# Kernel optimization log

Hardware: AMD Instinct MI355X
Metric: run time of the kernel (lower is better)

Reference implementation:

```python
import jax, jax.numpy as jnp
import numpy as np

B, IN, H, M = 16384, 512, 512, 4096


def setup_inputs() -> dict:
    key = jax.random.key(0)
    ks = jax.random.split(key, 8)
    s_in = 1.0 / np.sqrt(IN + H)
    return {
        "input_tensor": jax.random.normal(ks[0], (B, IN), jnp.float32),
        "hidden": jax.random.normal(ks[1], (B, H), jnp.float32),
        "cell": jax.random.normal(ks[2], (B, H), jnp.float32),
        # fused gate weights: columns = [input, forget, cell, output] gates
        "W_gates": jax.random.normal(ks[3], (IN + H, 4 * H), jnp.float32) * s_in,
        "b_gates": jnp.zeros((4 * H,), jnp.float32),
        "W_attn": jax.random.normal(ks[4], (H, M), jnp.float32) / np.sqrt(H),
        "b_attn": jnp.zeros((M,), jnp.float32),
        "memory_matrix": jax.random.normal(ks[5], (M, H), jnp.float32) * np.sqrt(2.0 / (M + H)),
    }


def reference(input_tensor, hidden, cell, W_gates, b_gates, W_attn, b_attn, memory_matrix):
    combined = jnp.concatenate([input_tensor, hidden], axis=1)        # (B, IN+H)
    gates = combined @ W_gates + b_gates                              # (B, 4H)
    i_g, f_g, c_g, o_g = jnp.split(gates, 4, axis=1)
    i_g = jax.nn.sigmoid(i_g)
    f_g = jax.nn.sigmoid(f_g)
    c_g = jnp.tanh(c_g)
    o_g = jax.nn.sigmoid(o_g)
    attn = jax.nn.softmax(hidden @ W_attn + b_attn, axis=1)           # (B, M)
    memory_read = attn @ memory_matrix                                # (B, H)
    new_cell = f_g * cell + i_g * c_g + 0.1 * memory_read
    new_hidden = o_g * jnp.tanh(new_cell)
    return (new_hidden, new_cell, attn)
```

## Files before the change

### kernel.cpp

```cpp
#include <hip/hip_runtime.h>
#include <hip/hip_bf16.h>
#include <math.h>

typedef __bf16 bf16_t;
typedef bf16_t bf16x8 __attribute__((ext_vector_type(8)));
typedef float  f32x4  __attribute__((ext_vector_type(4)));

static constexpr int Bn = 16384;
static constexpr int Hn = 512;

__device__ __forceinline__ float sigm(float x) { return 1.0f / (1.0f + __expf(-x)); }

typedef __attribute__((address_space(3))) void lds_void;
typedef const __attribute__((address_space(1))) void gl_void;

__device__ __forceinline__ void glds16(const void* g, void* l) {
    __builtin_amdgcn_global_load_lds((gl_void*)g, (lds_void*)l, 16, 0, 0);
}

__global__ void prologue(const float* __restrict__ inp, const float* __restrict__ hid,
                         bf16_t* __restrict__ comb,
                         const float* __restrict__ Wg, bf16_t* __restrict__ WgT,
                         const float* __restrict__ Wa, bf16_t* __restrict__ WaT,
                         const float* __restrict__ Mem, bf16_t* __restrict__ MemT)
{
    int b = blockIdx.x;
    if (b < 8192) {
        size_t t = (size_t)b * blockDim.x + threadIdx.x;
        size_t r = t >> 7;
        int c8 = (int)(t & 127);
        const float* src = (c8 < 64) ? (inp + r * 512 + c8 * 8) : (hid + r * 512 + (c8 - 64) * 8);
        float4 a = ((const float4*)src)[0];
        float4 bb = ((const float4*)src)[1];
        bf16x8 o;
        o[0] = (bf16_t)a.x; o[1] = (bf16_t)a.y; o[2] = (bf16_t)a.z; o[3] = (bf16_t)a.w;
        o[4] = (bf16_t)bb.x; o[5] = (bf16_t)bb.y; o[6] = (bf16_t)bb.z; o[7] = (bf16_t)bb.w;
        *(bf16x8*)(comb + t * 8) = o;
        return;
    }
    b -= 8192;
    __shared__ float tile[32][33];
    const float* src; bf16_t* dst; int R, C, gx;
    if (b < 2048)      { src = Wg;  dst = WgT;  R = 1024; C = 2048; gx = 64; }
    else if (b < 4096) { b -= 2048; src = Wa;  dst = WaT;  R = 512;  C = 4096; gx = 128; }
    else               { b -= 4096; src = Mem; dst = MemT; R = 4096; C = 512;  gx = 16; }
    const int x0 = (b % gx) * 32, y0 = (b / gx) * 32;
    const int tx = threadIdx.x & 31, ty = threadIdx.x >> 5;
#pragma unroll
    for (int i = 0; i < 32; i += 8)
        tile[ty + i][tx] = src[(size_t)(y0 + ty + i) * C + x0 + tx];
    __syncthreads();
#pragma unroll
    for (int i = 0; i < 32; i += 8)
        dst[(size_t)(x0 + ty + i) * R + y0 + tx] = (bf16_t)tile[tx][ty + i];
}

template<int EPI>
__global__ __launch_bounds__(512)
void gemm_w8(const bf16_t* __restrict__ A, int lda,
             const bf16_t* __restrict__ Bt, int ldb,
             const float* __restrict__ bias, int K, int N,
             bf16_t* __restrict__ bout, int ost)
{
    __shared__ __align__(16) bf16_t sA[128 * 64];
    __shared__ __align__(16) bf16_t sB[256 * 64];

    const int tid = threadIdx.x, lane = tid & 63, wid = tid >> 6;
    const int wr = wid >> 2, wc = wid & 3;

    const int nwg = gridDim.x;
    int bid = (blockIdx.x & 7) * (nwg >> 3) + (blockIdx.x >> 3);
    const int cbn = N >> 8;
    const int row0 = (bid / cbn) * 128, col0 = (bid % cbn) * 256;

    f32x4 acc[4][4] = {};
    const int nk = K >> 6;
    const int l15 = lane & 15, kq = lane >> 4;

    for (int kt = 0; kt < nk; ++kt) {
        const int k0 = kt << 6;
        {
            const int slot = (lane & 7) ^ (lane >> 3);
#pragma unroll
            for (int t = 0; t < 2; ++t) {
                const int c8 = wid * 2 + t;
                const int r = c8 * 8 + (lane >> 3);
                glds16(A + (size_t)(row0 + r) * lda + k0 + slot * 8, sA + c8 * 512);
            }
#pragma unroll
            for (int t = 0; t < 4; ++t) {
                const int c8 = wid * 4 + t;
                const int r = c8 * 8 + (lane >> 3);
                glds16(Bt + (size_t)(col0 + r) * ldb + k0 + slot * 8, sB + c8 * 512);
            }
        }
        __syncthreads();
#pragma unroll
        for (int ks = 0; ks < 2; ++ks) {
            bf16x8 af[4], bfr[4];
            const int slot = (ks * 4 + kq) ^ (l15 & 7);
#pragma unroll
            for (int j = 0; j < 4; ++j) {
                const int rb = wc * 64 + j * 16 + l15;
                bfr[j] = *(const bf16x8*)&sB[rb * 64 + slot * 8];
                const int ra = wr * 64 + j * 16 + l15;
                af[j] = *(const bf16x8*)&sA[ra * 64 + slot * 8];
            }
#pragma unroll
            for (int i = 0; i < 4; ++i)
#pragma unroll
                for (int j = 0; j < 4; ++j)
                    acc[i][j] = __builtin_amdgcn_mfma_f32_16x16x32_bf16(af[i], bfr[j], acc[i][j], 0, 0, 0);
        }
        __syncthreads();
    }

    const int lr = (lane >> 4) * 4, lc = lane & 15;
#pragma unroll
    for (int i = 0; i < 4; ++i) {
#pragma unroll
        for (int j = 0; j < 4; ++j) {
#pragma unroll
            for (int r = 0; r < 4; ++r) {
                const int grow = row0 + wr * 64 + i * 16 + lr + r;
                const int gcol = col0 + wc * 64 + j * 16 + lc;
                float v = acc[i][j][r] + bias[gcol];
                if constexpr (EPI == 0) {
                    const float a = ((gcol >> 9) == 2) ? tanhf(v) : sigm(v);
                    bout[(size_t)grow * 2048 + gcol] = (bf16_t)a;
                } else {
                    bout[(size_t)grow * ost + gcol] = (bf16_t)__expf(v);
                }
            }
        }
    }
}

__global__ __launch_bounds__(512)
void gemm3o(const bf16_t* __restrict__ E, int estride,
            const bf16_t* __restrict__ MemT,
            const bf16_t* __restrict__ gates, const float* __restrict__ cell,
            float* __restrict__ fout, float* __restrict__ denomBuf)
{
    __shared__ __align__(16) bf16_t sA[64 * 64];
    __shared__ __align__(16) bf16_t sB[256 * 64];

    const int tid = threadIdx.x, lane = tid & 63, wid = tid >> 6;
    const int wr = wid >> 2, wc = wid & 3;

    int bid = (blockIdx.x & 7) * 64 + (blockIdx.x >> 3);
    const int row0 = (bid >> 1) * 64, col0 = (bid & 1) * 256;

    f32x4 acc[2][4] = {};
    f32x4 dacc[2] = {};
    const int l15 = lane & 15, kq = lane >> 4;

    bf16x8 ones;
#pragma unroll
    for (int e = 0; e < 8; ++e) ones[e] = (bf16_t)1.0f;

    for (int kt = 0; kt < 64; ++kt) {
        const int k0 = kt << 6;
        const int slot = (lane & 7) ^ (lane >> 3);
        {
            const int c8 = wid;
            const int r = c8 * 8 + (lane >> 3);
            glds16(E + (size_t)(row0 + r) * estride + k0 + slot * 8, sA + c8 * 512);
        }
#pragma unroll
        for (int t = 0; t < 4; ++t) {
            const int c8 = wid * 4 + t;
            const int r = c8 * 8 + (lane >> 3);
            glds16(MemT + (size_t)(col0 + r) * 4096 + k0 + slot * 8, sB + c8 * 512);
        }
        __syncthreads();
#pragma unroll
        for (int ks = 0; ks < 2; ++ks) {
            bf16x8 af[2], bfr[4];
            const int sl = (ks * 4 + kq) ^ (l15 & 7);
#pragma unroll
            for (int j = 0; j < 4; ++j) {
                const int rb = wc * 64 + j * 16 + l15;
                bfr[j] = *(const bf16x8*)&sB[rb * 64 + sl * 8];
            }
#pragma unroll
            for (int i = 0; i < 2; ++i) {
                const int ra = wr * 32 + i * 16 + l15;
                af[i] = *(const bf16x8*)&sA[ra * 64 + sl * 8];
            }
#pragma unroll
            for (int i = 0; i < 2; ++i) {
#pragma unroll
                for (int j = 0; j < 4; ++j)
                    acc[i][j] = __builtin_amdgcn_mfma_f32_16x16x32_bf16(af[i], bfr[j], acc[i][j], 0, 0, 0);
                dacc[i] = __builtin_amdgcn_mfma_f32_16x16x32_bf16(af[i], ones, dacc[i], 0, 0, 0);
            }
        }
        __syncthreads();
    }

    const int lr = (lane >> 4) * 4, lc = lane & 15;

    if (col0 == 0 && wc == 0 && l15 == 0) {
#pragma unroll
        for (int i = 0; i < 2; ++i)
#pragma unroll
            for (int r = 0; r < 4; ++r)
                denomBuf[row0 + wr * 32 + i * 16 + lr + r] = dacc[i][r];
    }

    float invd[2][4];
#pragma unroll
    for (int i = 0; i < 2; ++i)
#pragma unroll
        for (int r = 0; r < 4; ++r) invd[i][r] = 1.0f / dacc[i][r];

#pragma unroll
    for (int i = 0; i < 2; ++i) {
#pragma unroll
        for (int j = 0; j < 4; ++j) {
#pragma unroll
            for (int r = 0; r < 4; ++r) {
                const int grow = row0 + wr * 32 + i * 16 + lr + r;
                const int gcol = col0 + wc * 64 + j * 16 + lc;
                const float v = acc[i][j][r] * invd[i][r];
                const float ig = (float)gates[(size_t)grow * 2048 + gcol];
                const float fg = (float)gates[(size_t)grow * 2048 + 512 + gcol];
                const float cg = (float)gates[(size_t)grow * 2048 + 1024 + gcol];
                const float og = (float)gates[(size_t)grow * 2048 + 1536 + gcol];
                const float cv = cell[(size_t)grow * 512 + gcol];
                const float ncv = fg * cv + ig * cg + 0.1f * v;
                fout[(size_t)grow * 512 + gcol] = og * tanhf(ncv);
                fout[(size_t)Bn * Hn + (size_t)grow * 512 + gcol] = ncv;
            }
        }
    }
}

__global__ __launch_bounds__(512)
void attn_writer(const bf16_t* __restrict__ E, int estride,
                 const float* __restrict__ denom, float* __restrict__ attn)
{
    const int row = blockIdx.x * 2 + (threadIdx.x >> 8);
    const int t = threadIdx.x & 255;
    const bf16_t* lp = E + (size_t)row * estride;
    const float inv = 1.0f / denom[row];
    bf16x8 a = ((const bf16x8*)lp)[2 * t];
    bf16x8 b = ((const bf16x8*)lp)[2 * t + 1];
    __syncthreads();
    float* rp = attn + (size_t)row * 4096;
    float4 o0 = { (float)a[0] * inv, (float)a[1] * inv, (float)a[2] * inv, (float)a[3] * inv };
    float4 o1 = { (float)a[4] * inv, (float)a[5] * inv, (float)a[6] * inv, (float)a[7] * inv };
    float4 o2 = { (float)b[0] * inv, (float)b[1] * inv, (float)b[2] * inv, (float)b[3] * inv };
    float4 o3 = { (float)b[4] * inv, (float)b[5] * inv, (float)b[6] * inv, (float)b[7] * inv };
    ((float4*)rp)[4 * t]     = o0;
    ((float4*)rp)[4 * t + 1] = o1;
    ((float4*)rp)[4 * t + 2] = o2;
    ((float4*)rp)[4 * t + 3] = o3;
}

extern "C" void kernel_launch(void* const* d_in, const int* in_sizes, int n_in,
                              void* d_out, int out_size, void* d_ws, size_t ws_size,
                              hipStream_t stream)
{
    const float* input  = (const float*)d_in[0];
    const float* hidden = (const float*)d_in[1];
    const float* cell   = (const float*)d_in[2];
    const float* Wg     = (const float*)d_in[3];
    const float* bg     = (const float*)d_in[4];
    const float* Wa     = (const float*)d_in[5];
    const float* ba     = (const float*)d_in[6];
    const float* Mem    = (const float*)d_in[7];

    float* out  = (float*)d_out;
    float* attn = out + 2ull * Bn * Hn;

    bf16_t* comb  = (bf16_t*)d_ws;
    bf16_t* WgT   = comb + (size_t)Bn * 1024;
    bf16_t* WaT   = WgT + (size_t)2048 * 1024;
    bf16_t* MemT  = WaT + (size_t)4096 * 512;
    bf16_t* gates = MemT + (size_t)512 * 4096;
    float*  denom = (float*)(gates + (size_t)Bn * 2048);
    bf16_t* pws   = (bf16_t*)(denom + Bn);

    const size_t need_big = (size_t)((char*)(pws + (size_t)Bn * 4096) - (char*)d_ws);
    const bool big = ws_size >= need_big;
    bf16_t* Ebuf = big ? pws : (bf16_t*)attn;
    const int estride = big ? 4096 : 8192;

    prologue<<<14336, 256, 0, stream>>>(input, hidden, comb, Wg, WgT, Wa, WaT, Mem, MemT);

    gemm_w8<1><<<2048, 512, 0, stream>>>(comb + 512, 1024, WaT, 512, ba, 512, 4096,
                                         Ebuf, estride);
    gemm_w8<0><<<1024, 512, 0, stream>>>(comb, 1024, WgT, 1024, bg, 1024, 2048, gates, 2048);

    gemm3o<<<512, 512, 0, stream>>>(Ebuf, estride, MemT, gates, cell, out, denom);

    attn_writer<<<8192, 512, 0, stream>>>(Ebuf, estride, denom, attn);
}
```

Before: 422.0 us.

## Compute softmax denominators in the logits GEMM and fuse attn write into gemm3o

The attention-logits GEMM epilogue now accumulates per-row partial sums of exp values, which a small reduce kernel turns into reciprocal denominators. gemm3o reads these instead of running extra ones-vector MFMAs, and when the large workspace is available it writes the normalized fp32 attn output straight from the E tiles already staged in LDS, alternating k-tiles between the two column blocks. This removes the separate attn_writer pass and its re-read of E, at the cost of an extra launch, a partial-sum buffer, and global stores interleaved with the MFMA loop.

```diff
diff --git a/kernel.cpp b/kernel.cpp
--- a/kernel.cpp
+++ b/kernel.cpp
@@ -60,7 +60,7 @@
 void gemm_w8(const bf16_t* __restrict__ A, int lda,
              const bf16_t* __restrict__ Bt, int ldb,
              const float* __restrict__ bias, int K, int N,
-             bf16_t* __restrict__ bout, int ost)
+             bf16_t* __restrict__ bout, int ost, float* __restrict__ dpart)
 {
     __shared__ __align__(16) bf16_t sA[128 * 64];
     __shared__ __align__(16) bf16_t sB[256 * 64];
@@ -116,6 +116,7 @@
     }
 
     const int lr = (lane >> 4) * 4, lc = lane & 15;
+    float s[4][4] = {};
 #pragma unroll
     for (int i = 0; i < 4; ++i) {
 #pragma unroll
@@ -129,35 +130,73 @@
                     const float a = ((gcol >> 9) == 2) ? tanhf(v) : sigm(v);
                     bout[(size_t)grow * 2048 + gcol] = (bf16_t)a;
                 } else {
-                    bout[(size_t)grow * ost + gcol] = (bf16_t)__expf(v);
+                    const float e = __expf(v);
+                    bout[(size_t)grow * ost + gcol] = (bf16_t)e;
+                    s[i][r] += e;
                 }
             }
         }
     }
+
+    if constexpr (EPI == 1) {
+#pragma unroll
+        for (int i = 0; i < 4; ++i)
+#pragma unroll
+            for (int r = 0; r < 4; ++r) {
+                float x = s[i][r];
+                x += __shfl_xor(x, 1); x += __shfl_xor(x, 2);
+                x += __shfl_xor(x, 4); x += __shfl_xor(x, 8);
+                s[i][r] = x;
+            }
+        float* sdnm = (float*)sA;
+        if (l15 == 0) {
+#pragma unroll
+            for (int i = 0; i < 4; ++i)
+#pragma unroll
+                for (int r = 0; r < 4; ++r)
+                    sdnm[(wr * 4 + wc) * 64 + i * 16 + kq * 4 + r] = s[i][r];
+        }
+        __syncthreads();
+        if (tid < 128) {
+            const int rw = tid & 63, w2 = tid >> 6;
+            const float p = sdnm[(w2 * 4 + 0) * 64 + rw] + sdnm[(w2 * 4 + 1) * 64 + rw]
+                          + sdnm[(w2 * 4 + 2) * 64 + rw] + sdnm[(w2 * 4 + 3) * 64 + rw];
+            dpart[(size_t)(col0 >> 8) * Bn + row0 + w2 * 64 + rw] = p;
+        }
+    }
+}
+
+__global__ void denom_reduce(const float* __restrict__ dpart, float* __restrict__ dinv)
+{
+    const int idx = blockIdx.x * 256 + threadIdx.x;
+    float s = 0.0f;
+#pragma unroll
+    for (int p = 0; p < 16; ++p) s += dpart[(size_t)p * Bn + idx];
+    dinv[idx] = 1.0f / s;
 }
 
 __global__ __launch_bounds__(512)
 void gemm3o(const bf16_t* __restrict__ E, int estride,
             const bf16_t* __restrict__ MemT,
             const bf16_t* __restrict__ gates, const float* __restrict__ cell,
-            float* __restrict__ fout, float* __restrict__ denomBuf)
+            float* __restrict__ fout, const float* __restrict__ dinv,
+            float* __restrict__ attnOut)
 {
     __shared__ __align__(16) bf16_t sA[64 * 64];
     __shared__ __align__(16) bf16_t sB[256 * 64];
+    __shared__ float sInvd[64];
 
     const int tid = threadIdx.x, lane = tid & 63, wid = tid >> 6;
     const int wr = wid >> 2, wc = wid & 3;
 
     int bid = (blockIdx.x & 7) * 64 + (blockIdx.x >> 3);
     const int row0 = (bid >> 1) * 64, col0 = (bid & 1) * 256;
+    const int oddsel = (col0 != 0) ? 1 : 0;
+
+    if (tid < 64) sInvd[tid] = dinv[row0 + tid];
 
     f32x4 acc[2][4] = {};
-    f32x4 dacc[2] = {};
     const int l15 = lane & 15, kq = lane >> 4;
-
-    bf16x8 ones;
-#pragma unroll
-    for (int e = 0; e < 8; ++e) ones[e] = (bf16_t)1.0f;
 
     for (int kt = 0; kt < 64; ++kt) {
         const int k0 = kt << 6;
@@ -189,31 +228,33 @@
                 af[i] = *(const bf16x8*)&sA[ra * 64 + sl * 8];
             }
 #pragma unroll
-            for (int i = 0; i < 2; ++i) {
+            for (int i = 0; i < 2; ++i)
 #pragma unroll
                 for (int j = 0; j < 4; ++j)
                     acc[i][j] = __builtin_amdgcn_mfma_f32_16x16x32_bf16(af[i], bfr[j], acc[i][j], 0, 0, 0);
-                dacc[i] = __builtin_amdgcn_mfma_f32_16x16x32_bf16(af[i], ones, dacc[i], 0, 0, 0);
-            }
+        }
+        if (attnOut && (kt & 1) == oddsel) {
+            const int rr = tid >> 3, sl8 = tid & 7;
+            const int koff = ((sl8 ^ (rr & 7)) << 3);
+            bf16x8 e8 = *(const bf16x8*)&sA[rr * 64 + sl8 * 8];
+            const float inv = sInvd[rr];
+            float* rp = attnOut + (size_t)(row0 + rr) * 4096 + k0 + koff;
+            float4 o0 = { (float)e8[0] * inv, (float)e8[1] * inv,
+                          (float)e8[2] * inv, (float)e8[3] * inv };
+            float4 o1 = { (float)e8[4] * inv, (float)e8[5] * inv,
+                          (float)e8[6] * inv, (float)e8[7] * inv };
+            *(float4*)rp = o0;
+            *((float4*)rp + 1) = o1;
         }
         __syncthreads();
     }
 
     const int lr = (lane >> 4) * 4, lc = lane & 15;
-
-    if (col0 == 0 && wc == 0 && l15 == 0) {
-#pragma unroll
-        for (int i = 0; i < 2; ++i)
-#pragma unroll
-            for (int r = 0; r < 4; ++r)
-                denomBuf[row0 + wr * 32 + i * 16 + lr + r] = dacc[i][r];
-    }
-
     float invd[2][4];
 #pragma unroll
     for (int i = 0; i < 2; ++i)
 #pragma unroll
-        for (int r = 0; r < 4; ++r) invd[i][r] = 1.0f / dacc[i][r];
+        for (int r = 0; r < 4; ++r) invd[i][r] = sInvd[wr * 32 + i * 16 + lr + r];
 
 #pragma unroll
     for (int i = 0; i < 2; ++i) {
@@ -239,12 +280,12 @@
 
 __global__ __launch_bounds__(512)
 void attn_writer(const bf16_t* __restrict__ E, int estride,
-                 const float* __restrict__ denom, float* __restrict__ attn)
+                 const float* __restrict__ dinv, float* __restrict__ attn)
 {
     const int row = blockIdx.x * 2 + (threadIdx.x >> 8);
     const int t = threadIdx.x & 255;
     const bf16_t* lp = E + (size_t)row * estride;
-    const float inv = 1.0f / denom[row];
+    const float inv = dinv[row];
     bf16x8 a = ((const bf16x8*)lp)[2 * t];
     bf16x8 b = ((const bf16x8*)lp)[2 * t + 1];
     __syncthreads();
@@ -280,8 +321,9 @@
     bf16_t* WaT   = WgT + (size_t)2048 * 1024;
     bf16_t* MemT  = WaT + (size_t)4096 * 512;
     bf16_t* gates = MemT + (size_t)512 * 4096;
-    float*  denom = (float*)(gates + (size_t)Bn * 2048);
-    bf16_t* pws   = (bf16_t*)(denom + Bn);
+    float*  dinv  = (float*)(gates + (size_t)Bn * 2048);
+    float*  dpart = dinv + Bn;
+    bf16_t* pws   = (bf16_t*)(dpart + 16 * (size_t)Bn);
 
     const size_t need_big = (size_t)((char*)(pws + (size_t)Bn * 4096) - (char*)d_ws);
     const bool big = ws_size >= need_big;
@@ -291,10 +333,14 @@
     prologue<<<14336, 256, 0, stream>>>(input, hidden, comb, Wg, WgT, Wa, WaT, Mem, MemT);
 
     gemm_w8<1><<<2048, 512, 0, stream>>>(comb + 512, 1024, WaT, 512, ba, 512, 4096,
-                                         Ebuf, estride);
-    gemm_w8<0><<<1024, 512, 0, stream>>>(comb, 1024, WgT, 1024, bg, 1024, 2048, gates, 2048);
-
-    gemm3o<<<512, 512, 0, stream>>>(Ebuf, estride, MemT, gates, cell, out, denom);
-
-    attn_writer<<<8192, 512, 0, stream>>>(Ebuf, estride, denom, attn);
-}
+                                         Ebuf, estride, dpart);
+    gemm_w8<0><<<1024, 512, 0, stream>>>(comb, 1024, WgT, 1024, bg, 1024, 2048,
+                                         gates, 2048, nullptr);
+
+    denom_reduce<<<64, 256, 0, stream>>>(dpart, dinv);
+
+    gemm3o<<<512, 512, 0, stream>>>(Ebuf, estride, MemT, gates, cell, out, dinv,
+                                    big ? attn : nullptr);
+
+    if (!big) attn_writer<<<8192, 512, 0, stream>>>(Ebuf, estride, dinv, attn);
+}
```

New measurement: 440.8 us. 4.5% more time.
